# Kernel optimization log

Measured on AMD Instinct MI355X. Metric: run time of the kernel, lower is better.

## Reference

```python
import jax, jax.numpy as jnp
import numpy as np

N, E, D, H, FF = 50000, 1600000, 128, 8, 512
DK = D // H
EPS = 1e-5


def _layernorm(x, g, b):
    mu = jnp.mean(x, axis=-1, keepdims=True)
    var = jnp.mean((x - mu) ** 2, axis=-1, keepdims=True)
    return (x - mu) * jax.lax.rsqrt(var + EPS) * g + b


def setup_inputs() -> dict:
    key = jax.random.key(0)
    ks = jax.random.split(key, 10)
    s = 0.05
    return {
        "h": jax.random.normal(ks[0], (N, D), jnp.float32),
        "src": jax.random.randint(ks[1], (E,), 0, N, jnp.int32),
        "dst": jax.random.randint(ks[2], (E,), 0, N, jnp.int32),
        "Wq": jax.random.normal(ks[3], (D, D), jnp.float32) * s,
        "Wk": jax.random.normal(ks[4], (D, D), jnp.float32) * s,
        "Wv": jax.random.normal(ks[5], (D, D), jnp.float32) * s,
        "Wo": jax.random.normal(ks[6], (D, D), jnp.float32) * s,
        "ln1_g": jnp.ones((D,), jnp.float32),
        "ln1_b": jnp.zeros((D,), jnp.float32),
        "ln2_g": jnp.ones((D,), jnp.float32),
        "ln2_b": jnp.zeros((D,), jnp.float32),
        "W1": jax.random.normal(ks[7], (D, FF), jnp.float32) * s,
        "b1": jnp.zeros((FF,), jnp.float32),
        "W2": jax.random.normal(ks[8], (FF, D), jnp.float32) * s,
        "b2": jnp.zeros((D,), jnp.float32),
    }


def reference(h, src, dst, Wq, Wk, Wv, Wo, ln1_g, ln1_b, ln2_g, ln2_b, W1, b1, W2, b2):
    # QKV projections (bias-free, as in the torch module)
    q = (h @ Wq).reshape(N, H, DK)
    k = (h @ Wk).reshape(N, H, DK)
    v = (h @ Wv).reshape(N, H, DK)

    # masked_mm: per-edge, per-head score  e[m,h] = q[dst[m]] . k[src[m]]
    e = jnp.einsum("ehd,ehd->eh", q[dst], k[src]) / np.sqrt(DK)

    # sparse_softmax: segment softmax over incoming edges of each dst node
    m = jax.ops.segment_max(e, dst, num_segments=N)  # [N, H]
    ex = jnp.exp(e - m[dst])
    denom = jax.ops.segment_sum(ex, dst, num_segments=N)  # [N, H]
    alpha = ex / denom[dst]  # [E, H]

    # vec_spmm: a[n] = sum_{edges m with dst[m]==n} alpha[m] * v[src[m]]
    a = jax.ops.segment_sum(alpha[:, :, None] * v[src], dst, num_segments=N)
    a = a.reshape(N, D)

    o = a @ Wo
    h1 = _layernorm(h + o, ln1_g, ln1_b)
    ffn = jax.nn.relu(h1 @ W1 + b1) @ W2 + b2
    h2 = _layernorm(h1 + ffn, ln2_g, ln2_b)
    return h2
```

## Files before the change

kernel.cpp:

```cpp
#include <hip/hip_runtime.h>
#include <hip/hip_bf16.h>
#include <math.h>

#define D   128
#define FFD 512
#define NPART 8
#define BINB 1024
#define BCAP 768
#define NPROD 32
#define NSUB 32
#define RCAP 320

typedef __attribute__((ext_vector_type(8))) short bf16x8;
typedef __attribute__((ext_vector_type(4))) float f32x4;
typedef __attribute__((ext_vector_type(2))) float f32x2;

static inline size_t align256(size_t x){ return (x + 255) & ~(size_t)255; }

__device__ __forceinline__ float bf2f(unsigned short u){
    union { unsigned int i; float f; } x; x.i = ((unsigned int)u) << 16; return x.f;
}
__device__ __forceinline__ unsigned short f2bf(float f){
    return __builtin_bit_cast(unsigned short, __float2bfloat16(f));
}
__device__ __forceinline__ unsigned char f2fp8(float f){
    return (unsigned char)(__builtin_amdgcn_cvt_pk_fp8_f32(f, f, 0, false) & 0xff);
}

#define DPP_ADD(x, ctrl) do { \
    int yi_ = __builtin_amdgcn_update_dpp(0, __builtin_bit_cast(int, x), ctrl, 0xf, 0xf, true); \
    x += __builtin_bit_cast(float, yi_); } while(0)

__global__ __launch_bounds__(256) void k_bin3(const int* __restrict__ src,
                                              const int* __restrict__ dst, int E, int N,
                                              unsigned long long* __restrict__ pairs,
                                              int* __restrict__ lens,
                                              unsigned long long* __restrict__ spill,
                                              int* __restrict__ qspill){
    __shared__ int lcur[8];
    int tid = threadIdx.x;
    if (tid < 8) lcur[tid] = 0;
    __syncthreads();
    int slice = (N + 7) >> 3;
    int T = gridDim.x * 256;
    unsigned long long* myreg = pairs + (size_t)blockIdx.x * 8 * BCAP;
    for (int i = blockIdx.x*256 + tid; i < E; i += T){
        int d = __builtin_nontemporal_load(&dst[i]);
        int s = __builtin_nontemporal_load(&src[i]);
        int b = min(d / slice, 7);
        unsigned long long pr = ((unsigned long long)(unsigned)d << 32) | (unsigned)s;
        int slot = atomicAdd(&lcur[b], 1);
        if (slot < BCAP) myreg[(size_t)b*BCAP + slot] = pr;
        else { int p = atomicAdd(qspill, 1); spill[p] = pr; }
    }
    __syncthreads();
    if (tid < 8) lens[blockIdx.x*8 + tid] = min(lcur[tid], BCAP);
}

__global__ __launch_bounds__(256) void k_rebin(const unsigned long long* __restrict__ pairs,
                                               const int* __restrict__ lens,
                                               unsigned* __restrict__ pairs2,
                                               int* __restrict__ rlens,
                                               unsigned long long* __restrict__ spill,
                                               int* __restrict__ qspill, int N){
    __shared__ int lcur[NSUB];
    int part = blockIdx.x & 7, ip = blockIdx.x >> 3;
    int tid = threadIdx.x;
    if (tid < NSUB) lcur[tid] = 0;
    __syncthreads();
    int slice = (N + 7) >> 3;
    unsigned subslice = (unsigned)(slice + NSUB - 1) / NSUB;
    int lo_part = part * slice;
    unsigned* outbase = pairs2 + (size_t)(part*NPROD + ip) * NSUB * RCAP;
    for (int seg = ip*(BINB/NPROD); seg < (ip+1)*(BINB/NPROD); ++seg){
        int len = lens[seg*8 + part];
        const unsigned long long* pp = pairs + ((size_t)seg*8 + part)*BCAP;
        for (int i = tid; i < len; i += 256){
            unsigned long long pr = pp[i];
            int d = (int)(pr >> 32);
            unsigned dl = (unsigned)(d - lo_part);
            unsigned sb = dl / subslice;
            int slot = atomicAdd(&lcur[sb], 1);
            if (slot < RCAP)
                outbase[(size_t)sb*RCAP + slot] = ((dl - sb*subslice) << 24) | (unsigned)pr & 0xFFFFFFu;
            else { int p = atomicAdd(qspill, 1); spill[p] = pr; }
        }
    }
    __syncthreads();
    if (tid < NSUB) rlens[(part*NPROD + ip)*NSUB + tid] = min(lcur[tid], RCAP);
}

__global__ __launch_bounds__(256) void k_count4(const unsigned* __restrict__ pairs2,
                                                const int* __restrict__ rlens,
                                                const unsigned long long* __restrict__ spill,
                                                const int* __restrict__ qspill,
                                                int* __restrict__ cnt, int N){
    __shared__ int hist[256];
    int part = blockIdx.x & 7, s = blockIdx.x >> 3;
    int slice = (N + 7) >> 3;
    int subslice = (slice + NSUB - 1) / NSUB;
    int lo_part = part*slice;
    int lo = lo_part + s*subslice;
    int part_end = min(lo_part + slice, N);
    int n_sub = max(0, min(subslice, part_end - lo));
    for (int i = threadIdx.x; i < 256; i += 256) hist[i] = 0;
    __syncthreads();
    for (int ip = 0; ip < NPROD; ++ip){
        int r = (part*NPROD + ip)*NSUB + s;
        int len = rlens[r];
        const unsigned* pp = pairs2 + (size_t)r*RCAP;
        for (int i = threadIdx.x; i < len; i += 256)
            atomicAdd(&hist[pp[i] >> 24], 1);
    }
    int ns = *qspill;
    for (int i = threadIdx.x; i < ns; i += 256){
        int r = (int)(spill[i] >> 32) - lo;
        if (r >= 0 && r < n_sub) atomicAdd(&hist[r], 1);
    }
    __syncthreads();
    for (int i = threadIdx.x; i < n_sub; i += 256) cnt[lo + i] = hist[i];
}

__global__ __launch_bounds__(256) void k_scatter4(const unsigned* __restrict__ pairs2,
                                                  const int* __restrict__ rlens,
                                                  const unsigned long long* __restrict__ spill,
                                                  const int* __restrict__ qspill,
                                                  const int* __restrict__ off,
                                                  int* __restrict__ csr_src, int N){
    __shared__ int curl[256];
    int part = blockIdx.x & 7, s = blockIdx.x >> 3;
    int slice = (N + 7) >> 3;
    int subslice = (slice + NSUB - 1) / NSUB;
    int lo_part = part*slice;
    int lo = lo_part + s*subslice;
    int part_end = min(lo_part + slice, N);
    int n_sub = max(0, min(subslice, part_end - lo));
    for (int i = threadIdx.x; i < n_sub; i += 256) curl[i] = off[lo + i];
    __syncthreads();
    for (int ip = 0; ip < NPROD; ++ip){
        int r = (part*NPROD + ip)*NSUB + s;
        int len = rlens[r];
        const unsigned* pp = pairs2 + (size_t)r*RCAP;
        for (int i = threadIdx.x; i < len; i += 256){
            unsigned e = pp[i];
            int pos = atomicAdd(&curl[e >> 24], 1);
            csr_src[pos] = (int)(e & 0xFFFFFFu);
        }
    }
    int ns = *qspill;
    for (int i = threadIdx.x; i < ns; i += 256){
        unsigned long long pr = spill[i];
        int r = (int)(pr >> 32) - lo;
        if (r >= 0 && r < n_sub){
            int pos = atomicAdd(&curl[r], 1);
            csr_src[pos] = (int)(unsigned)pr;
        }
    }
}

__global__ __launch_bounds__(256) void k_bsum(const int* __restrict__ cnt, int N,
                                              int* __restrict__ bsum){
    int id = blockIdx.x*256 + threadIdx.x;
    int v = (id < N) ? cnt[id] : 0;
    #pragma unroll
    for (int o = 1; o < 64; o <<= 1) v += __shfl_xor(v, o);
    __shared__ int w4[4];
    if ((threadIdx.x & 63) == 0) w4[threadIdx.x >> 6] = v;
    __syncthreads();
    if (threadIdx.x == 0) bsum[blockIdx.x] = w4[0] + w4[1] + w4[2] + w4[3];
}

__global__ __launch_bounds__(1024) void k_scanb(const int* __restrict__ bsum, int NB,
                                                int* __restrict__ ebase,
                                                int* __restrict__ off, int N){
    __shared__ int sh[1024];
    int tid = threadIdx.x;
    int v = (tid < NB) ? bsum[tid] : 0;
    sh[tid] = v; __syncthreads();
    for (int o = 1; o < 1024; o <<= 1){
        int t = (tid >= o) ? sh[tid-o] : 0;
        __syncthreads();
        sh[tid] += t;
        __syncthreads();
    }
    if (tid < NB) ebase[tid] = sh[tid] - v;
    if (tid == NB-1) off[N] = sh[tid];
}

__global__ __launch_bounds__(256) void k_off(const int* __restrict__ cnt, int N,
                                             const int* __restrict__ ebase,
                                             int* __restrict__ off){
    __shared__ int sh[256];
    int tid = threadIdx.x;
    int id = blockIdx.x*256 + tid;
    int v = (id < N) ? cnt[id] : 0;
    sh[tid] = v; __syncthreads();
    for (int o = 1; o < 256; o <<= 1){
        int t = (tid >= o) ? sh[tid-o] : 0;
        __syncthreads();
        sh[tid] += t;
        __syncthreads();
    }
    int excl = sh[tid] - v;
    int base = ebase[blockIdx.x];
    if (id < N) off[id] = base + excl;
}

__global__ __launch_bounds__(256) void k_cast(const float* __restrict__ x,
                                              __hip_bfloat16* __restrict__ y, int n4){
    int i = blockIdx.x*blockDim.x + threadIdx.x;
    if (i >= n4) return;
    float4 f = ((const float4*)x)[i];
    ushort4 u;
    u.x = f2bf(f.x); u.y = f2bf(f.y);
    u.z = f2bf(f.z); u.w = f2bf(f.w);
    ((ushort4*)y)[i] = u;
}

__global__ __launch_bounds__(256) void k_prep_all(
    const float* __restrict__ Wq, const float* __restrict__ Wk,
    const float* __restrict__ Wv, const float* __restrict__ Wo,
    const float* __restrict__ W1, const float* __restrict__ W2,
    __hip_bfloat16* __restrict__ Wqkvt, __hip_bfloat16* __restrict__ Wot,
    __hip_bfloat16* __restrict__ W1t,   __hip_bfloat16* __restrict__ W2t){
    const float* W; __hip_bfloat16* Wt; int K, Nc;
    int y = blockIdx.y;
    switch (y){
        case 0: W = Wq; Wt = Wqkvt; K = 128; Nc = 128; break;
        case 1: W = Wk; Wt = Wqkvt; K = 128; Nc = 128; break;
        case 2: W = Wv; Wt = Wqkvt; K = 128; Nc = 128; break;
        case 3: W = Wo; Wt = Wot;   K = 128; Nc = 128; break;
        case 4: W = W1; Wt = W1t;   K = 128; Nc = 512; break;
        default: W = W2; Wt = W2t;  K = 512; Nc = 128; break;
    }
    int total = K*Nc;
    for (int id = blockIdx.x*256 + threadIdx.x; id < total; id += 256*gridDim.x){
        int n = id / K, kk = id % K;
        size_t drow;
        if (y == 1)      drow = 128 + 8*(n>>2) + (n&3);
        else if (y == 2) drow = 128 + 8*(n>>2) + 4 + (n&3);
        else             drow = n;
        Wt[drow*K + kk] = __float2bfloat16(W[(size_t)kk*Nc + n]);
    }
}

#define BM 128
#define BN 128
#define BK 64

__device__ __forceinline__ bool tile_coords(int M, int &r0, int &c0){
    int ncols = gridDim.x;
    int f = blockIdx.y * ncols + blockIdx.x;
    int xcd = f & 7, s = f >> 3;
    int c = s % ncols, rl = s / ncols;
    int r = rl*8 + xcd;
    r0 = r*BM; c0 = c*BN;
    return r0 < M;
}

__device__ __forceinline__ void stage_tile(const __hip_bfloat16* __restrict__ src,
                                           int row_base, int row_limit, int K, int k0,
                                           __hip_bfloat16* lds){
    int tid = threadIdx.x;
    int wave = tid >> 6;
    #pragma unroll
    for (int i = 0; i < 4; ++i){
        int c = i*256 + tid;
        int r = c >> 3, s = c & 7;
        int sg = s ^ (r & 7);
        int gr = row_base + r; if (gr >= row_limit) gr = row_limit - 1;
        const __hip_bfloat16* gp = src + (size_t)gr*K + k0 + sg*8;
        char* lp = (char*)lds + (i*256 + wave*64)*16;
        __builtin_amdgcn_global_load_lds((const __attribute__((address_space(1))) void*)gp,
                                         (__attribute__((address_space(3))) void*)lp,
                                         16, 0, 0);
    }
}

template<int MODE>
__global__ __launch_bounds__(256) void k_gemm(
    const __hip_bfloat16* __restrict__ A,
    const __hip_bfloat16* __restrict__ Bt,
    int M, int Nc, int K,
    const float* __restrict__ bias, int relu,
    __hip_bfloat16* __restrict__ Cb,
    __hip_bfloat16* __restrict__ qb, unsigned char* __restrict__ kvq,
    const float* __restrict__ resid_f, const __hip_bfloat16* __restrict__ resid_b,
    const float* __restrict__ lg, const float* __restrict__ lb,
    float* __restrict__ yf, __hip_bfloat16* __restrict__ yb){
    __shared__ __hip_bfloat16 As[BM*BK];
    __shared__ __hip_bfloat16 Bs[BN*BK];
    __shared__ float red[2][BM][2];
    int r0, c0;
    if (!tile_coords(M, r0, c0)) return;
    int tid = threadIdx.x;
    int lane = tid & 63, wave = tid >> 6;
    int wr = wave >> 1, wc = wave & 1;
    int lr = lane & 15, ls = lane >> 4;

    f32x4 acc[4][4];
    #pragma unroll
    for (int m = 0; m < 4; m++)
        #pragma unroll
        for (int n = 0; n < 4; n++) acc[m][n] = (f32x4){0.f,0.f,0.f,0.f};

    for (int k0 = 0; k0 < K; k0 += BK){
        stage_tile(A,  r0, M,  K, k0, As);
        stage_tile(Bt, c0, Nc, K, k0, Bs);
        __syncthreads();
        #pragma unroll
        for (int kk = 0; kk < 2; ++kk){
            bf16x8 af[4], bfg[4];
            #pragma unroll
            for (int m = 0; m < 4; m++){
                int R = wr*64 + m*16 + lr;
                int sl = (kk*4 + ls) ^ (R & 7);
                af[m] = *(const bf16x8*)((const char*)As + R*128 + sl*16);
            }
            #pragma unroll
            for (int n = 0; n < 4; n++){
                int R = wc*64 + n*16 + lr;
                int sl = (kk*4 + ls) ^ (R & 7);
                bfg[n] = *(const bf16x8*)((const char*)Bs + R*128 + sl*16);
            }
            #pragma unroll
            for (int m = 0; m < 4; m++)
                #pragma unroll
                for (int n = 0; n < 4; n++)
                    acc[m][n] = __builtin_amdgcn_mfma_f32_16x16x32_bf16(af[m], bfg[n], acc[m][n], 0, 0, 0);
        }
        __syncthreads();
    }

    if (MODE == 0){
        #pragma unroll
        for (int n = 0; n < 4; n++){
            int col = c0 + wc*64 + n*16 + lr;
            float bval = bias ? bias[col] : 0.f;
            #pragma unroll
            for (int m = 0; m < 4; m++){
                #pragma unroll
                for (int j = 0; j < 4; j++){
                    int row = r0 + wr*64 + m*16 + ls*4 + j;
                    if (row >= M) continue;
                    float v = acc[m][n][j] + bval;
                    if (relu) v = fmaxf(v, 0.f);
                    Cb[(size_t)row*Nc + col] = __float2bfloat16(v);
                }
            }
        }
    } else if (MODE == 1){
        int region = c0 >> 7;
        #pragma unroll
        for (int n = 0; n < 4; n++){
            int c16 = wc*64 + n*16 + lr;
            #pragma unroll
            for (int m = 0; m < 4; m++){
                #pragma unroll
                for (int j = 0; j < 4; j++){
                    int row = r0 + wr*64 + m*16 + ls*4 + j;
                    if (row >= M) continue;
                    float v = acc[m][n][j];
                    if (region == 0)
                        ((unsigned short*)qb)[(size_t)row*128 + c16] = f2bf(v);
                    else
                        kvq[(size_t)row*256 + (region-1)*128 + c16] = f2fp8(v);
                }
            }
        }
    } else {
        #pragma unroll
        for (int m = 0; m < 4; m++){
            #pragma unroll
            for (int j = 0; j < 4; j++){
                int row = r0 + wr*64 + m*16 + ls*4 + j;
                float s = 0.f, q = 0.f;
                if (row < M){
                    #pragma unroll
                    for (int n = 0; n < 4; n++){
                        int col = wc*64 + n*16 + lr;
                        float bval = bias ? bias[col] : 0.f;
                        float rv = (MODE == 2) ? resid_f[(size_t)row*128 + col]
                                               : bf2f(((const unsigned short*)resid_b)[(size_t)row*128 + col]);
                        float v = acc[m][n][j] + bval + rv;
                        acc[m][n][j] = v;
                        s += v; q += v*v;
                    }
                }
                #pragma unroll
                for (int o = 1; o < 16; o <<= 1){
                    s += __shfl_xor(s, o);
                    q += __shfl_xor(q, o);
                }
                if (lr == 0 && row < M){
                    int rloc = wr*64 + m*16 + ls*4 + j;
                    red[0][rloc][wc] = s;
                    red[1][rloc][wc] = q;
                }
            }
        }
        __syncthreads();
        #pragma unroll
        for (int m = 0; m < 4; m++){
            #pragma unroll
            for (int j = 0; j < 4; j++){
                int rloc = wr*64 + m*16 + ls*4 + j;
                int row = r0 + rloc;
                if (row >= M) continue;
                float mu  = (red[0][rloc][0] + red[0][rloc][1]) * (1.f/128.f);
                float eq  = (red[1][rloc][0] + red[1][rloc][1]) * (1.f/128.f);
                float var = fmaxf(eq - mu*mu, 0.f);
                float inv = rsqrtf(var + 1e-5f);
                #pragma unroll
                for (int n = 0; n < 4; n++){
                    int col = wc*64 + n*16 + lr;
                    float o = (acc[m][n][j] - mu)*inv*lg[col] + lb[col];
                    if (MODE == 3) yf[(size_t)row*128 + col] = o;
                    else           yb[(size_t)row*128 + col] = __float2bfloat16(o);
                }
            }
        }
    }
}

#define PAIR(jj, dd, b0, b1, b2, b3) { \
    int s0_ = __builtin_amdgcn_readlane(myidx, (jj)); \
    int s1_ = __builtin_amdgcn_readlane(myidx, (jj)+1); \
    int sv_ = half ? s1_ : s0_; \
    uint2 u_ = kv[(size_t)(unsigned)sv_*32 + l32]; \
    f32x2 k01 = __builtin_amdgcn_cvt_pk_f32_fp8((int)u_.x, false); \
    f32x2 k23 = __builtin_amdgcn_cvt_pk_f32_fp8((int)u_.x, true); \
    f32x2 v01 = __builtin_amdgcn_cvt_pk_f32_fp8((int)u_.y, false); \
    f32x2 v23 = __builtin_amdgcn_cvt_pk_f32_fp8((int)u_.y, true); \
    float p_ = q0*k01[0] + q1*k01[1] + q2*k23[0] + q3*k23[1]; \
    DPP_ADD(p_, 0xB1); DPP_ADD(p_, 0x4E); \
    float w_ = __builtin_amdgcn_exp2f(p_); \
    dd += w_; \
    b0 = fmaf(w_, v01[0], b0); b1 = fmaf(w_, v01[1], b1); \
    b2 = fmaf(w_, v23[0], b2); b3 = fmaf(w_, v23[1], b3); }

#define PAIRV(jj, dd, b0, b1, b2, b3) { \
    int s0_ = __builtin_amdgcn_readlane(myidx, (jj)); \
    int s1_ = __builtin_amdgcn_readlane(myidx, min((jj)+1, 63)); \
    int sv_ = half ? s1_ : s0_; \
    uint2 u_ = kv[(size_t)(unsigned)sv_*32 + l32]; \
    f32x2 k01 = __builtin_amdgcn_cvt_pk_f32_fp8((int)u_.x, false); \
    f32x2 k23 = __builtin_amdgcn_cvt_pk_f32_fp8((int)u_.x, true); \
    f32x2 v01 = __builtin_amdgcn_cvt_pk_f32_fp8((int)u_.y, false); \
    f32x2 v23 = __builtin_amdgcn_cvt_pk_f32_fp8((int)u_.y, true); \
    float p_ = q0*k01[0] + q1*k01[1] + q2*k23[0] + q3*k23[1]; \
    DPP_ADD(p_, 0xB1); DPP_ADD(p_, 0x4E); \
    float w_ = __builtin_amdgcn_exp2f(p_); \
    if ((jj) + half >= cnt) w_ = 0.f; \
    dd += w_; \
    b0 = fmaf(w_, v01[0], b0); b1 = fmaf(w_, v01[1], b1); \
    b2 = fmaf(w_, v23[0], b2); b3 = fmaf(w_, v23[1], b3); }

__global__ __launch_bounds__(256) void k_attn(const __hip_bfloat16* __restrict__ qb,
                                              const uint2* __restrict__ kv,
                                              const int* __restrict__ off,
                                              const int* __restrict__ csr_src,
                                              __hip_bfloat16* __restrict__ a, int N){
    int wid = (blockIdx.x*blockDim.x + threadIdx.x) >> 6;
    int lane = threadIdx.x & 63;
    if (wid >= N) return;
    int half = lane >> 5, l32 = lane & 31;
    ushort4 qu = ((const ushort4*)(qb + (size_t)wid*128))[l32];
    const float SC = 0.25f * 1.44269504f;
    float q0 = bf2f(qu.x)*SC, q1 = bf2f(qu.y)*SC, q2 = bf2f(qu.z)*SC, q3 = bf2f(qu.w)*SC;
    int beg = off[wid], end = off[wid+1];
    float dA=0, a0A=0, a1A=0, a2A=0, a3A=0;
    float dB=0, a0B=0, a1B=0, a2B=0, a3B=0;
    for (int e0 = beg; e0 < end; e0 += 64){
        int myidx = (e0 + lane < end) ? csr_src[e0 + lane] : 0;
        int cnt = min(64, end - e0);
        int j = 0;
        for (; j + 3 < cnt; j += 4){
            PAIR(j,   dA, a0A, a1A, a2A, a3A);
            PAIR(j+2, dB, a0B, a1B, a2B, a3B);
        }
        for (; j < cnt; j += 2){
            PAIRV(j, dA, a0A, a1A, a2A, a3A);
        }
    }
    float d  = dA + dB;
    float a0 = a0A + a0B, a1 = a1A + a1B, a2 = a2A + a2B, a3 = a3A + a3B;
    d  += __shfl_xor(d, 32);
    a0 += __shfl_xor(a0, 32);
    a1 += __shfl_xor(a1, 32);
    a2 += __shfl_xor(a2, 32);
    a3 += __shfl_xor(a3, 32);
    if (half == 0){
        float r = (d > 0.f) ? 1.f/d : 0.f;
        ushort4 o;
        o.x = f2bf(a0*r); o.y = f2bf(a1*r); o.z = f2bf(a2*r); o.w = f2bf(a3*r);
        ((ushort4*)(a + (size_t)wid*128))[l32] = o;
    }
}

extern "C" void kernel_launch(void* const* d_in, const int* in_sizes, int n_in,
                              void* d_out, int out_size, void* d_ws, size_t ws_size,
                              hipStream_t stream){
    const float* h    = (const float*)d_in[0];
    const int*   src  = (const int*)  d_in[1];
    const int*   dst  = (const int*)  d_in[2];
    const float* Wq   = (const float*)d_in[3];
    const float* Wk   = (const float*)d_in[4];
    const float* Wv   = (const float*)d_in[5];
    const float* Wo   = (const float*)d_in[6];
    const float* ln1g = (const float*)d_in[7];
    const float* ln1b = (const float*)d_in[8];
    const float* ln2g = (const float*)d_in[9];
    const float* ln2b = (const float*)d_in[10];
    const float* W1   = (const float*)d_in[11];
    const float* b1   = (const float*)d_in[12];
    const float* W2   = (const float*)d_in[13];
    const float* b2   = (const float*)d_in[14];
    float* out = (float*)d_out;

    const int N = in_sizes[0] / D;
    const int E = in_sizes[1];

    char* ws = (char*)d_ws;
    size_t o = 0;
    const size_t row_bf = align256((size_t)N * D * sizeof(__hip_bfloat16));
    const size_t kv_q   = align256((size_t)N * 256);
    const size_t t1_bf  = align256((size_t)N * FFD * sizeof(__hip_bfloat16));

    __hip_bfloat16* qb  = (__hip_bfloat16*)(ws + o); o += row_bf;
    unsigned char* kvq  = (unsigned char*)(ws + o); o += kv_q;
    __hip_bfloat16* ab  = (__hip_bfloat16*)(ws + o); o += row_bf;
    __hip_bfloat16* hb  = (__hip_bfloat16*)(ws + o); o += row_bf;
    __hip_bfloat16* h1b = hb;
    __hip_bfloat16* t1b = (__hip_bfloat16*)(ws + o); o += t1_bf;
    __hip_bfloat16* Wqkvt = (__hip_bfloat16*)(ws + o); o += align256(384*128*2);
    __hip_bfloat16* W1t   = (__hip_bfloat16*)(ws + o); o += align256(512*128*2);
    __hip_bfloat16* W2t   = (__hip_bfloat16*)(ws + o); o += align256(128*512*2);
    __hip_bfloat16* Wot   = (__hip_bfloat16*)(ws + o); o += align256(128*128*2);
    int* cnt   = (int*)(ws + o); o += align256((size_t)N*4);
    int* offp  = (int*)(ws + o); o += align256((size_t)(N+1)*4);
    int* bsum  = (int*)(ws + o); o += align256(1024*4);
    int* ebase = (int*)(ws + o); o += align256(1024*4);
    int* lens  = (int*)(ws + o); o += align256((size_t)BINB*8*4);
    int* rlens = (int*)(ws + o); o += align256((size_t)NPART*NPROD*NSUB*4);
    int* qspill= (int*)(ws + o); o += align256(256);
    int* csr   = (int*)(ws + o); o += align256((size_t)E*4);
    unsigned long long* pairs = (unsigned long long*)(ws + o);
    o += align256((size_t)BINB * 8 * BCAP * 8);
    unsigned* pairs2 = (unsigned*)(ws + o);
    o += align256((size_t)NPART * NPROD * NSUB * RCAP * 4);
    unsigned long long* spill = (unsigned long long*)(ws + o);
    o += align256((size_t)E * 8);

    const int NB = (N + 255)/256;

    (void)hipMemsetAsync(qspill, 0, 256, stream);
    k_bin3<<<BINB, 256, 0, stream>>>(src, dst, E, N, pairs, lens, spill, qspill);

    k_cast<<<(N*D/4 + 255)/256, 256, 0, stream>>>(h, hb, N*D/4);
    k_prep_all<<<dim3(64, 6), 256, 0, stream>>>(Wq, Wk, Wv, Wo, W1, W2,
                                                Wqkvt, Wot, W1t, W2t);

    k_rebin<<<NPART*NPROD, 256, 0, stream>>>(pairs, lens, pairs2, rlens, spill, qspill, N);
    k_count4<<<NPART*NSUB, 256, 0, stream>>>(pairs2, rlens, spill, qspill, cnt, N);
    k_bsum <<<NB, 256, 0, stream>>>(cnt, N, bsum);
    k_scanb<<<1, 1024, 0, stream>>>(bsum, NB, ebase, offp, N);
    k_off  <<<NB, 256, 0, stream>>>(cnt, N, ebase, offp);
    k_scatter4<<<NPART*NSUB, 256, 0, stream>>>(pairs2, rlens, spill, qspill, offp, csr, N);

    int mb = (N + BM - 1)/BM;
    int mb_pad = ((mb + 7)/8)*8;

    k_gemm<1><<<dim3(3, mb_pad), 256, 0, stream>>>(hb, Wqkvt, N, 384, 128,
        nullptr, 0, nullptr, qb, kvq, nullptr, nullptr, nullptr, nullptr, nullptr, nullptr);

    k_attn<<<(N*64 + 255)/256, 256, 0, stream>>>(qb, (const uint2*)kvq, offp, csr, ab, N);

    k_gemm<2><<<dim3(1, mb_pad), 256, 0, stream>>>(ab, Wot, N, 128, 128,
        nullptr, 0, nullptr, nullptr, nullptr, h, nullptr, ln1g, ln1b, nullptr, h1b);

    k_gemm<0><<<dim3(4, mb_pad), 256, 0, stream>>>(h1b, W1t, N, 512, 128,
        b1, 1, t1b, nullptr, nullptr, nullptr, nullptr, nullptr, nullptr, nullptr, nullptr);

    k_gemm<3><<<dim3(1, mb_pad), 256, 0, stream>>>(t1b, W2t, N, 128, 512,
        b2, 0, nullptr, nullptr, nullptr, nullptr, h1b, ln2g, ln2b, out, nullptr);
}
```

Baseline: 242.3 us.

## Fuse output projection, LayerNorms and FFN into one per-row-tile kernel

Replaces the three tail GEMM launches (Wo+LN1, W1+ReLU, W2+LN2) with a single kernel in which each block owns a 128-row tile. The block keeps h1 and chunks of the FFN hidden activation in LDS instead of writing them to global memory. This removes the N×512 bf16 intermediate round trip and the h1 round trip, plus two launches. In exchange it uses more LDS per block (about 80KB), which lowers occupancy. Each block also has only one block per row tile, about 400 blocks in total, and runs the weight staging serially with no overlap.

```diff
diff --git a/kernel.cpp b/kernel.cpp
--- a/kernel.cpp
+++ b/kernel.cpp
@@ -259,7 +259,7 @@
 }
 
 __device__ __forceinline__ void stage_tile(const __hip_bfloat16* __restrict__ src,
-                                           int row_base, int row_limit, int K, int k0,
+                                           int row_base, int row_limit, int ldK, int k0,
                                            __hip_bfloat16* lds){
     int tid = threadIdx.x;
     int wave = tid >> 6;
@@ -269,7 +269,7 @@
         int r = c >> 3, s = c & 7;
         int sg = s ^ (r & 7);
         int gr = row_base + r; if (gr >= row_limit) gr = row_limit - 1;
-        const __hip_bfloat16* gp = src + (size_t)gr*K + k0 + sg*8;
+        const __hip_bfloat16* gp = src + (size_t)gr*ldK + k0 + sg*8;
         char* lp = (char*)lds + (i*256 + wave*64)*16;
         __builtin_amdgcn_global_load_lds((const __attribute__((address_space(1))) void*)gp,
                                          (__attribute__((address_space(3))) void*)lp,
@@ -277,20 +277,18 @@
     }
 }
 
-template<int MODE>
-__global__ __launch_bounds__(256) void k_gemm(
+__device__ __forceinline__ bf16x8 frag(const __hip_bfloat16* buf, int R, int kk, int ls){
+    int sl = (kk*4 + ls) ^ (R & 7);
+    return *(const bf16x8*)((const char*)buf + R*128 + sl*16);
+}
+
+__global__ __launch_bounds__(256) void k_gemm_qkv(
     const __hip_bfloat16* __restrict__ A,
     const __hip_bfloat16* __restrict__ Bt,
-    int M, int Nc, int K,
-    const float* __restrict__ bias, int relu,
-    __hip_bfloat16* __restrict__ Cb,
-    __hip_bfloat16* __restrict__ qb, unsigned char* __restrict__ kvq,
-    const float* __restrict__ resid_f, const __hip_bfloat16* __restrict__ resid_b,
-    const float* __restrict__ lg, const float* __restrict__ lb,
-    float* __restrict__ yf, __hip_bfloat16* __restrict__ yb){
+    int M,
+    __hip_bfloat16* __restrict__ qb, unsigned char* __restrict__ kvq){
     __shared__ __hip_bfloat16 As[BM*BK];
     __shared__ __hip_bfloat16 Bs[BN*BK];
-    __shared__ float red[2][BM][2];
     int r0, c0;
     if (!tile_coords(M, r0, c0)) return;
     int tid = threadIdx.x;
@@ -304,25 +302,17 @@
         #pragma unroll
         for (int n = 0; n < 4; n++) acc[m][n] = (f32x4){0.f,0.f,0.f,0.f};
 
-    for (int k0 = 0; k0 < K; k0 += BK){
-        stage_tile(A,  r0, M,  K, k0, As);
-        stage_tile(Bt, c0, Nc, K, k0, Bs);
+    for (int k0 = 0; k0 < 128; k0 += BK){
+        stage_tile(A,  r0, M,   128, k0, As);
+        stage_tile(Bt, c0, 384, 128, k0, Bs);
         __syncthreads();
         #pragma unroll
         for (int kk = 0; kk < 2; ++kk){
             bf16x8 af[4], bfg[4];
             #pragma unroll
-            for (int m = 0; m < 4; m++){
-                int R = wr*64 + m*16 + lr;
-                int sl = (kk*4 + ls) ^ (R & 7);
-                af[m] = *(const bf16x8*)((const char*)As + R*128 + sl*16);
-            }
-            #pragma unroll
-            for (int n = 0; n < 4; n++){
-                int R = wc*64 + n*16 + lr;
-                int sl = (kk*4 + ls) ^ (R & 7);
-                bfg[n] = *(const bf16x8*)((const char*)Bs + R*128 + sl*16);
-            }
+            for (int m = 0; m < 4; m++) af[m]  = frag(As, wr*64 + m*16 + lr, kk, ls);
+            #pragma unroll
+            for (int n = 0; n < 4; n++) bfg[n] = frag(Bs, wc*64 + n*16 + lr, kk, ls);
             #pragma unroll
             for (int m = 0; m < 4; m++)
                 #pragma unroll
@@ -332,92 +322,230 @@
         __syncthreads();
     }
 
-    if (MODE == 0){
-        #pragma unroll
-        for (int n = 0; n < 4; n++){
-            int col = c0 + wc*64 + n*16 + lr;
-            float bval = bias ? bias[col] : 0.f;
-            #pragma unroll
-            for (int m = 0; m < 4; m++){
-                #pragma unroll
-                for (int j = 0; j < 4; j++){
-                    int row = r0 + wr*64 + m*16 + ls*4 + j;
-                    if (row >= M) continue;
-                    float v = acc[m][n][j] + bval;
-                    if (relu) v = fmaxf(v, 0.f);
-                    Cb[(size_t)row*Nc + col] = __float2bfloat16(v);
-                }
-            }
-        }
-    } else if (MODE == 1){
-        int region = c0 >> 7;
-        #pragma unroll
-        for (int n = 0; n < 4; n++){
-            int c16 = wc*64 + n*16 + lr;
-            #pragma unroll
-            for (int m = 0; m < 4; m++){
-                #pragma unroll
-                for (int j = 0; j < 4; j++){
-                    int row = r0 + wr*64 + m*16 + ls*4 + j;
-                    if (row >= M) continue;
-                    float v = acc[m][n][j];
-                    if (region == 0)
-                        ((unsigned short*)qb)[(size_t)row*128 + c16] = f2bf(v);
-                    else
-                        kvq[(size_t)row*256 + (region-1)*128 + c16] = f2fp8(v);
-                }
-            }
-        }
-    } else {
+    int region = c0 >> 7;
+    #pragma unroll
+    for (int n = 0; n < 4; n++){
+        int c16 = wc*64 + n*16 + lr;
         #pragma unroll
         for (int m = 0; m < 4; m++){
             #pragma unroll
             for (int j = 0; j < 4; j++){
                 int row = r0 + wr*64 + m*16 + ls*4 + j;
-                float s = 0.f, q = 0.f;
-                if (row < M){
+                if (row >= M) continue;
+                float v = acc[m][n][j];
+                if (region == 0)
+                    ((unsigned short*)qb)[(size_t)row*128 + c16] = f2bf(v);
+                else
+                    kvq[(size_t)row*256 + (region-1)*128 + c16] = f2fp8(v);
+            }
+        }
+    }
+}
+
+__global__ __launch_bounds__(256) void k_tail(
+    const __hip_bfloat16* __restrict__ ab, const float* __restrict__ h,
+    const __hip_bfloat16* __restrict__ Wot,
+    const float* __restrict__ ln1g, const float* __restrict__ ln1b,
+    const __hip_bfloat16* __restrict__ W1t, const float* __restrict__ b1,
+    const __hip_bfloat16* __restrict__ W2t, const float* __restrict__ b2,
+    const float* __restrict__ ln2g, const float* __restrict__ ln2b,
+    float* __restrict__ out, int M){
+    __shared__ __hip_bfloat16 As[BM*BK];
+    __shared__ __hip_bfloat16 Bs[BM*BK];
+    __shared__ __hip_bfloat16 h1s[2][BM*BK];
+    __shared__ __hip_bfloat16 t1s[2][BM*BK];
+    __shared__ float red[2][BM][2];
+    int f = blockIdx.x;
+    int r0 = ((f >> 3)*8 + (f & 7)) * BM;
+    if (r0 >= M) return;
+    int tid = threadIdx.x;
+    int lane = tid & 63, wave = tid >> 6;
+    int wr = wave >> 1, wc = wave & 1;
+    int lr = lane & 15, ls = lane >> 4;
+
+    f32x4 acc[4][4];
+    #pragma unroll
+    for (int m = 0; m < 4; m++)
+        #pragma unroll
+        for (int n = 0; n < 4; n++) acc[m][n] = (f32x4){0.f,0.f,0.f,0.f};
+
+    for (int k0 = 0; k0 < 128; k0 += BK){
+        stage_tile(ab,  r0, M,   128, k0, As);
+        stage_tile(Wot, 0,  128, 128, k0, Bs);
+        __syncthreads();
+        #pragma unroll
+        for (int kk = 0; kk < 2; ++kk){
+            bf16x8 af[4], bfg[4];
+            #pragma unroll
+            for (int m = 0; m < 4; m++) af[m]  = frag(As, wr*64 + m*16 + lr, kk, ls);
+            #pragma unroll
+            for (int n = 0; n < 4; n++) bfg[n] = frag(Bs, wc*64 + n*16 + lr, kk, ls);
+            #pragma unroll
+            for (int m = 0; m < 4; m++)
+                #pragma unroll
+                for (int n = 0; n < 4; n++)
+                    acc[m][n] = __builtin_amdgcn_mfma_f32_16x16x32_bf16(af[m], bfg[n], acc[m][n], 0, 0, 0);
+        }
+        __syncthreads();
+    }
+
+    #pragma unroll
+    for (int m = 0; m < 4; m++){
+        #pragma unroll
+        for (int j = 0; j < 4; j++){
+            int rowl = wr*64 + m*16 + ls*4 + j;
+            int row = r0 + rowl;
+            float s = 0.f, q = 0.f;
+            #pragma unroll
+            for (int n = 0; n < 4; n++){
+                int col = wc*64 + n*16 + lr;
+                float rv = (row < M) ? h[(size_t)row*128 + col] : 0.f;
+                float v = acc[m][n][j] + rv;
+                acc[m][n][j] = v;
+                s += v; q += v*v;
+            }
+            #pragma unroll
+            for (int o = 1; o < 16; o <<= 1){
+                s += __shfl_xor(s, o);
+                q += __shfl_xor(q, o);
+            }
+            if (lr == 0){
+                red[0][rowl][wc] = s;
+                red[1][rowl][wc] = q;
+            }
+        }
+    }
+    __syncthreads();
+    #pragma unroll
+    for (int m = 0; m < 4; m++){
+        #pragma unroll
+        for (int j = 0; j < 4; j++){
+            int rowl = wr*64 + m*16 + ls*4 + j;
+            float mu  = (red[0][rowl][0] + red[0][rowl][1]) * (1.f/128.f);
+            float eq  = (red[1][rowl][0] + red[1][rowl][1]) * (1.f/128.f);
+            float var = fmaxf(eq - mu*mu, 0.f);
+            float inv = rsqrtf(var + 1e-5f);
+            #pragma unroll
+            for (int n = 0; n < 4; n++){
+                int col = wc*64 + n*16 + lr;
+                float o = (acc[m][n][j] - mu)*inv*ln1g[col] + ln1b[col];
+                int half = col >> 6, c6 = col & 63;
+                int slot = (c6 >> 3) ^ (rowl & 7), elem = c6 & 7;
+                ((unsigned short*)h1s[half])[rowl*64 + slot*8 + elem] = f2bf(o);
+            }
+        }
+    }
+    __syncthreads();
+
+    f32x4 yacc[4][4];
+    #pragma unroll
+    for (int m = 0; m < 4; m++)
+        #pragma unroll
+        for (int n = 0; n < 4; n++) yacc[m][n] = (f32x4){0.f,0.f,0.f,0.f};
+
+    for (int c = 0; c < 4; ++c){
+        f32x4 tacc[4][4];
+        #pragma unroll
+        for (int m = 0; m < 4; m++)
+            #pragma unroll
+            for (int n = 0; n < 4; n++) tacc[m][n] = (f32x4){0.f,0.f,0.f,0.f};
+        for (int step = 0; step < 2; ++step){
+            stage_tile(W1t, c*128, 512, 128, step*64, Bs);
+            __syncthreads();
+            #pragma unroll
+            for (int kk = 0; kk < 2; ++kk){
+                bf16x8 af[4], bfg[4];
+                #pragma unroll
+                for (int m = 0; m < 4; m++) af[m]  = frag(h1s[step], wr*64 + m*16 + lr, kk, ls);
+                #pragma unroll
+                for (int n = 0; n < 4; n++) bfg[n] = frag(Bs, wc*64 + n*16 + lr, kk, ls);
+                #pragma unroll
+                for (int m = 0; m < 4; m++)
                     #pragma unroll
-                    for (int n = 0; n < 4; n++){
-                        int col = wc*64 + n*16 + lr;
-                        float bval = bias ? bias[col] : 0.f;
-                        float rv = (MODE == 2) ? resid_f[(size_t)row*128 + col]
-                                               : bf2f(((const unsigned short*)resid_b)[(size_t)row*128 + col]);
-                        float v = acc[m][n][j] + bval + rv;
-                        acc[m][n][j] = v;
-                        s += v; q += v*v;
-                    }
-                }
-                #pragma unroll
-                for (int o = 1; o < 16; o <<= 1){
-                    s += __shfl_xor(s, o);
-                    q += __shfl_xor(q, o);
-                }
-                if (lr == 0 && row < M){
-                    int rloc = wr*64 + m*16 + ls*4 + j;
-                    red[0][rloc][wc] = s;
-                    red[1][rloc][wc] = q;
-                }
-            }
-        }
-        __syncthreads();
+                    for (int n = 0; n < 4; n++)
+                        tacc[m][n] = __builtin_amdgcn_mfma_f32_16x16x32_bf16(af[m], bfg[n], tacc[m][n], 0, 0, 0);
+            }
+            __syncthreads();
+        }
         #pragma unroll
         for (int m = 0; m < 4; m++){
             #pragma unroll
             for (int j = 0; j < 4; j++){
-                int rloc = wr*64 + m*16 + ls*4 + j;
-                int row = r0 + rloc;
-                if (row >= M) continue;
-                float mu  = (red[0][rloc][0] + red[0][rloc][1]) * (1.f/128.f);
-                float eq  = (red[1][rloc][0] + red[1][rloc][1]) * (1.f/128.f);
-                float var = fmaxf(eq - mu*mu, 0.f);
-                float inv = rsqrtf(var + 1e-5f);
+                int rowl = wr*64 + m*16 + ls*4 + j;
                 #pragma unroll
                 for (int n = 0; n < 4; n++){
                     int col = wc*64 + n*16 + lr;
-                    float o = (acc[m][n][j] - mu)*inv*lg[col] + lb[col];
-                    if (MODE == 3) yf[(size_t)row*128 + col] = o;
-                    else           yb[(size_t)row*128 + col] = __float2bfloat16(o);
+                    float v = fmaxf(tacc[m][n][j] + b1[c*128 + col], 0.f);
+                    int half = col >> 6, c6 = col & 63;
+                    int slot = (c6 >> 3) ^ (rowl & 7), elem = c6 & 7;
+                    ((unsigned short*)t1s[half])[rowl*64 + slot*8 + elem] = f2bf(v);
                 }
+            }
+        }
+        __syncthreads();
+        for (int step = 0; step < 2; ++step){
+            stage_tile(W2t, 0, 128, 512, c*128 + step*64, Bs);
+            __syncthreads();
+            #pragma unroll
+            for (int kk = 0; kk < 2; ++kk){
+                bf16x8 af[4], bfg[4];
+                #pragma unroll
+                for (int m = 0; m < 4; m++) af[m]  = frag(t1s[step], wr*64 + m*16 + lr, kk, ls);
+                #pragma unroll
+                for (int n = 0; n < 4; n++) bfg[n] = frag(Bs, wc*64 + n*16 + lr, kk, ls);
+                #pragma unroll
+                for (int m = 0; m < 4; m++)
+                    #pragma unroll
+                    for (int n = 0; n < 4; n++)
+                        yacc[m][n] = __builtin_amdgcn_mfma_f32_16x16x32_bf16(af[m], bfg[n], yacc[m][n], 0, 0, 0);
+            }
+            __syncthreads();
+        }
+    }
+
+    #pragma unroll
+    for (int m = 0; m < 4; m++){
+        #pragma unroll
+        for (int j = 0; j < 4; j++){
+            int rowl = wr*64 + m*16 + ls*4 + j;
+            float s = 0.f, q = 0.f;
+            #pragma unroll
+            for (int n = 0; n < 4; n++){
+                int col = wc*64 + n*16 + lr;
+                int half = col >> 6, c6 = col & 63;
+                int slot = (c6 >> 3) ^ (rowl & 7), elem = c6 & 7;
+                float h1v = bf2f(((const unsigned short*)h1s[half])[rowl*64 + slot*8 + elem]);
+                float v = yacc[m][n][j] + b2[col] + h1v;
+                yacc[m][n][j] = v;
+                s += v; q += v*v;
+            }
+            #pragma unroll
+            for (int o = 1; o < 16; o <<= 1){
+                s += __shfl_xor(s, o);
+                q += __shfl_xor(q, o);
+            }
+            if (lr == 0){
+                red[0][rowl][wc] = s;
+                red[1][rowl][wc] = q;
+            }
+        }
+    }
+    __syncthreads();
+    #pragma unroll
+    for (int m = 0; m < 4; m++){
+        #pragma unroll
+        for (int j = 0; j < 4; j++){
+            int rowl = wr*64 + m*16 + ls*4 + j;
+            int row = r0 + rowl;
+            if (row >= M) continue;
+            float mu  = (red[0][rowl][0] + red[0][rowl][1]) * (1.f/128.f);
+            float eq  = (red[1][rowl][0] + red[1][rowl][1]) * (1.f/128.f);
+            float var = fmaxf(eq - mu*mu, 0.f);
+            float inv = rsqrtf(var + 1e-5f);
+            #pragma unroll
+            for (int n = 0; n < 4; n++){
+                int col = wc*64 + n*16 + lr;
+                out[(size_t)row*128 + col] = (yacc[m][n][j] - mu)*inv*ln2g[col] + ln2b[col];
             }
         }
     }
@@ -525,14 +653,11 @@
     size_t o = 0;
     const size_t row_bf = align256((size_t)N * D * sizeof(__hip_bfloat16));
     const size_t kv_q   = align256((size_t)N * 256);
-    const size_t t1_bf  = align256((size_t)N * FFD * sizeof(__hip_bfloat16));
 
     __hip_bfloat16* qb  = (__hip_bfloat16*)(ws + o); o += row_bf;
     unsigned char* kvq  = (unsigned char*)(ws + o); o += kv_q;
     __hip_bfloat16* ab  = (__hip_bfloat16*)(ws + o); o += row_bf;
     __hip_bfloat16* hb  = (__hip_bfloat16*)(ws + o); o += row_bf;
-    __hip_bfloat16* h1b = hb;
-    __hip_bfloat16* t1b = (__hip_bfloat16*)(ws + o); o += t1_bf;
     __hip_bfloat16* Wqkvt = (__hip_bfloat16*)(ws + o); o += align256(384*128*2);
     __hip_bfloat16* W1t   = (__hip_bfloat16*)(ws + o); o += align256(512*128*2);
     __hip_bfloat16* W2t   = (__hip_bfloat16*)(ws + o); o += align256(128*512*2);
@@ -571,17 +696,10 @@
     int mb = (N + BM - 1)/BM;
     int mb_pad = ((mb + 7)/8)*8;
 
-    k_gemm<1><<<dim3(3, mb_pad), 256, 0, stream>>>(hb, Wqkvt, N, 384, 128,
-        nullptr, 0, nullptr, qb, kvq, nullptr, nullptr, nullptr, nullptr, nullptr, nullptr);
+    k_gemm_qkv<<<dim3(3, mb_pad), 256, 0, stream>>>(hb, Wqkvt, N, qb, kvq);
 
     k_attn<<<(N*64 + 255)/256, 256, 0, stream>>>(qb, (const uint2*)kvq, offp, csr, ab, N);
 
-    k_gemm<2><<<dim3(1, mb_pad), 256, 0, stream>>>(ab, Wot, N, 128, 128,
-        nullptr, 0, nullptr, nullptr, nullptr, h, nullptr, ln1g, ln1b, nullptr, h1b);
-
-    k_gemm<0><<<dim3(4, mb_pad), 256, 0, stream>>>(h1b, W1t, N, 512, 128,
-        b1, 1, t1b, nullptr, nullptr, nullptr, nullptr, nullptr, nullptr, nullptr, nullptr);
-
-    k_gemm<3><<<dim3(1, mb_pad), 256, 0, stream>>>(t1b, W2t, N, 128, 512,
-        b2, 0, nullptr, nullptr, nullptr, nullptr, h1b, ln2g, ln2b, out, nullptr);
-}
+    k_tail<<<mb_pad, 256, 0, stream>>>(ab, h, Wot, ln1g, ln1b,
+                                       W1t, b1, W2t, b2, ln2g, ln2b, out, N);
+}
```

New measurement: 230.5 us. -4.9%, faster.
